# Kernel optimization log

Measured on AMD Instinct MI355X. Metric: run time of the kernel, lower is better.

Reference implementation:

```python
import jax, jax.numpy as jnp
import numpy as np

B, P = 65536, 22  # sets, max players per freeze frame
IN, HID, OUT = 6, 64, 128


def setup_inputs() -> dict:
    key = jax.random.key(0)
    k0, k1, k2, k3, k4, k5 = jax.random.split(key, 6)
    pitch = jnp.array([120.0, 80.0], dtype=jnp.float32)
    player_locs = jax.random.uniform(k0, (B, P, 2), dtype=jnp.float32) * pitch
    actor_locs = jax.random.uniform(k1, (B, 2), dtype=jnp.float32) * pitch
    # teammate / keeper flags in {0,1}
    flags = jax.random.randint(k2, (B, P, 2), 0, 2).astype(jnp.float32)
    # validity mask: 0 -> player skipped (simulates ragged / missing entries)
    mask = jax.random.randint(k3, (B, P), 0, 2).astype(jnp.int32)
    W1 = jax.random.normal(k4, (IN, HID), dtype=jnp.float32) / np.sqrt(IN)
    b1 = jnp.zeros((HID,), dtype=jnp.float32)
    W2 = jax.random.normal(k5, (HID, OUT), dtype=jnp.float32) / np.sqrt(HID)
    b2 = jnp.zeros((OUT,), dtype=jnp.float32)
    return {"player_locs": player_locs, "actor_locs": actor_locs, "flags": flags,
            "mask": mask, "W1": W1, "b1": b1, "W2": W2, "b2": b2}


def reference(player_locs, actor_locs, flags, mask, W1, b1, W2, b2):
    # per-player features relative to the actor: [dx, dy, dist, angle, teammate, keeper]
    dxy = player_locs - actor_locs[:, None, :]                 # [B,P,2]
    dist = jnp.sqrt(jnp.sum(dxy * dxy, axis=-1, keepdims=True))  # [B,P,1]
    angle = jnp.arctan2(dxy[..., 1:2], dxy[..., 0:1])            # [B,P,1]
    feats = jnp.concatenate([dxy, dist, angle, flags], axis=-1)  # [B,P,6]
    # PlayerMLP: Linear -> ReLU -> Linear
    h = jax.nn.relu(jnp.einsum('bpi,ih->bph', feats, W1) + b1)   # [B,P,64]
    emb = jnp.einsum('bph,ho->bpo', h, W2) + b2                  # [B,P,128]
    # masked mean over valid players; empty sets yield zeros (sum is 0)
    m = mask.astype(emb.dtype)[..., None]                        # [B,P,1]
    cnt = jnp.sum(m, axis=1)                                     # [B,1]
    pooled = jnp.sum(emb * m, axis=1) / jnp.maximum(cnt, 1.0)    # [B,128]
    return pooled
```

## Files before the change

### kernel.cpp

```cpp
#include <hip/hip_runtime.h>
#include <math.h>

#define PMAX 22
#define HID 64
#define OUTD 128
#define SETS_PER_WAVE 8
#define WAVES_PER_BLOCK 4

typedef __attribute__((ext_vector_type(4))) float float4v;
typedef _Float16 fh2 __attribute__((ext_vector_type(2)));
typedef _Float16 half8 __attribute__((ext_vector_type(8)));

__device__ __forceinline__ int rl_i(int v, int l) {
    return __builtin_amdgcn_readlane(v, l);
}
__device__ __forceinline__ int pk2(float x, float y) {
    auto v = __builtin_amdgcn_cvt_pkrtz(x, y);
    union { decltype(v) h; int i; } c;
    c.h = v;
    return c.i;
}
__device__ __forceinline__ unsigned short f16b(float x) {
    return (unsigned short)(pk2(x, x) & 0xFFFF);
}
__device__ __forceinline__ float fdot2i(int a, int b, float c) {
    union { int i; fh2 h; } ua, ub;
    ua.i = a;
    ub.i = b;
#if defined(__has_builtin) && __has_builtin(__builtin_amdgcn_fdot2)
    return __builtin_amdgcn_fdot2(ua.h, ub.h, c, false);
#else
    return fmaf((float)ua.h.x, (float)ub.h.x, fmaf((float)ua.h.y, (float)ub.h.y, c));
#endif
}
__device__ __forceinline__ void wave_lds_sync() {
    asm volatile("s_waitcnt lgkmcnt(0)" ::: "memory");
    __builtin_amdgcn_wave_barrier();
}
__device__ __forceinline__ float fast_atan2(float y, float x) {
    float ax = fabsf(x), ay = fabsf(y);
    float mn = fminf(ax, ay), mx = fmaxf(ax, ay);
    float a = mn * __builtin_amdgcn_rcpf(fmaxf(mx, 1e-30f));
    float s = a * a;
    float r = a * fmaf(s, fmaf(s, fmaf(s, -0.0851330f, 0.1801410f), -0.3302995f), 0.9998660f);
    if (ay > ax) r = 1.57079637f - r;
    if (x < 0.0f) r = 3.14159274f - r;
    return copysignf(r, y);
}

__global__ __launch_bounds__(256) void set_encoder_kernel(
    const float* __restrict__ player_locs,
    const float* __restrict__ actor_locs,
    const float* __restrict__ flags,
    const int*   __restrict__ mask,
    const float* __restrict__ W1,
    const float* __restrict__ b1,
    const float* __restrict__ W2,
    const float* __restrict__ b2,
    float* __restrict__ out)
{
    __shared__ __align__(16) unsigned w2f[16 * 256];
    __shared__ __align__(16) unsigned short hb[WAVES_PER_BLOCK][SETS_PER_WAVE][72];

    const int tid  = threadIdx.x;
    const int lane = tid & 63;
    const int wave = tid >> 6;

    const int wave_id = blockIdx.x * WAVES_PER_BLOCK + wave;
    const int set0    = wave_id * SETS_PER_WAVE;

    {
        const int pr = tid >> 3;
        const int nt = tid & 7;
        const float* rA = W2 + (size_t)(2 * pr) * OUTD + 16 * nt;
        const float* rB = rA + OUTD;
        float ra[16], rb[16];
#pragma unroll
        for (int i = 0; i < 4; ++i) {
            *(float4*)&ra[4 * i] = ((const float4*)rA)[i];
            *(float4*)&rb[4 * i] = ((const float4*)rB)[i];
        }
        const int kt = pr >> 4;
        const int kk = (2 * pr) & 31;
        const int Q  = kk >> 3;
        const int j2 = (kk >> 1) & 3;
        const int base = ((kt * 8 + nt) * 4 + Q) * 64 + j2;
#pragma unroll
        for (int c = 0; c < 16; ++c)
            w2f[base + 4 * c] = pk2(ra[c], rb[c]);
    }

    const int w01 = pk2(W1[0 * HID + lane], W1[1 * HID + lane]);
    const int w23 = pk2(W1[2 * HID + lane], W1[3 * HID + lane]);
    const int w45 = pk2(W1[4 * HID + lane], W1[5 * HID + lane]);
    const float b1l = b1[lane];

    __syncthreads();

    int fh[4][3];
    unsigned long long wbm[4];
    {
        const int lidx = lane < 2 * PMAX ? lane : 2 * PMAX - 1;
        const size_t r0 = (size_t)set0 * PMAX + lidx;
        const float2* plb = (const float2*)player_locs + r0;
        const float2* flb = (const float2*)flags + r0;
        const int*    mkb = mask + r0;
        const float2* acb = (const float2*)actor_locs + set0 + (lidx >= PMAX ? 1 : 0);
#pragma unroll
        for (int g = 0; g < 4; ++g) {
            float2 pl = plb[g * 2 * PMAX];
            float2 fl = flb[g * 2 * PMAX];
            int    m  = mkb[g * 2 * PMAX];
            float2 ac = acb[2 * g];
            float dx = pl.x - ac.x;
            float dy = pl.y - ac.y;
            float dist = __builtin_amdgcn_sqrtf(fmaf(dx, dx, dy * dy));
            float ang  = fast_atan2(dy, dx);
            fh[g][0] = pk2(dx, dy);
            fh[g][1] = pk2(dist, ang);
            fh[g][2] = pk2(fl.x, fl.y);
            unsigned long long bl = __ballot((lane < 2 * PMAX) && (m != 0));
            const unsigned lo = __builtin_amdgcn_readfirstlane((unsigned)bl);
            const unsigned hi = __builtin_amdgcn_readfirstlane((unsigned)(bl >> 32));
            wbm[g] = ((unsigned long long)hi << 32) | lo;
        }
    }

    unsigned nonempty = 0;
#pragma unroll
    for (int s = 0; s < SETS_PER_WAVE; ++s) {
        const int g    = s >> 1;
        const int base = (s & 1) * PMAX;
        const unsigned bits = (unsigned)(wbm[g] >> base) & 0x3FFFFFu;
        const int cnt = __builtin_popcount(bits);
        if (bits) nonempty |= (1u << s);
        float acc = 0.0f;
#pragma unroll
        for (int p = 0; p < PMAX; ++p) {
            if (bits & (1u << p)) {
                float t = fdot2i(rl_i(fh[g][0], base + p), w01, b1l);
                t = fdot2i(rl_i(fh[g][1], base + p), w23, t);
                t = fdot2i(rl_i(fh[g][2], base + p), w45, t);
                acc += fmaxf(t, 0.0f);
            }
        }
        const float hbar = acc * (1.0f / fmaxf((float)cnt, 1.0f));
        hb[wave][s][lane] = f16b(hbar);
    }
    wave_lds_sync();

    const int Q   = lane >> 4;
    const int c15 = lane & 15;
    const int sA  = lane & 7;
    half8 afrag[2];
#pragma unroll
    for (int kt = 0; kt < 2; ++kt) {
        union { uint4 u4; half8 h8; } cv;
        cv.u4 = *(const uint4*)&hb[wave][sA][kt * 32 + Q * 8];
        afrag[kt] = cv.h8;
    }

    float4v acc[8];
#pragma unroll
    for (int nt = 0; nt < 8; ++nt) {
        union { uint4 u4; half8 h8; } f0, f1;
        f0.u4 = *(const uint4*)&w2f[(0 * 8 + nt) * 256 + 4 * lane];
        f1.u4 = *(const uint4*)&w2f[(1 * 8 + nt) * 256 + 4 * lane];
        float4v z = {0.0f, 0.0f, 0.0f, 0.0f};
        acc[nt] = __builtin_amdgcn_mfma_f32_16x16x32_f16(afrag[0], f0.h8, z, 0, 0, 0);
        acc[nt] = __builtin_amdgcn_mfma_f32_16x16x32_f16(afrag[1], f1.h8, acc[nt], 0, 0, 0);
    }

    if (Q < 2) {
        float fs[4];
#pragma unroll
        for (int r = 0; r < 4; ++r) fs[r] = (float)((nonempty >> (4 * Q + r)) & 1u);

        const float* b2b = b2 + c15;
        float b2v[8];
#pragma unroll
        for (int nt = 0; nt < 8; ++nt) b2v[nt] = b2b[16 * nt];

        float* obase = out + (size_t)(set0 + 4 * Q) * OUTD + c15;
#pragma unroll
        for (int nt = 0; nt < 8; ++nt) {
#pragma unroll
            for (int r = 0; r < 4; ++r)
                obase[r * OUTD + nt * 16] = fmaf(fs[r], b2v[nt], acc[nt][r]);
        }
    }
}

extern "C" void kernel_launch(void* const* d_in, const int* in_sizes, int n_in,
                              void* d_out, int out_size, void* d_ws, size_t ws_size,
                              hipStream_t stream) {
    const float* player_locs = (const float*)d_in[0];
    const float* actor_locs  = (const float*)d_in[1];
    const float* flags       = (const float*)d_in[2];
    const int*   mask        = (const int*)d_in[3];
    const float* W1          = (const float*)d_in[4];
    const float* b1          = (const float*)d_in[5];
    const float* W2          = (const float*)d_in[6];
    const float* b2          = (const float*)d_in[7];
    float*       out         = (float*)d_out;

    const int B = in_sizes[0] / (PMAX * 2);
    const int sets_per_block = WAVES_PER_BLOCK * SETS_PER_WAVE;
    const int grid = (B + sets_per_block - 1) / sets_per_block;

    hipLaunchKernelGGL(set_encoder_kernel, dim3(grid), dim3(256), 0, stream,
                       player_locs, actor_locs, flags, mask, W1, b1, W2, b2, out);
}
```

Measured before the change: 110.4 us.

## Process two set groups per wave with prefetch of next group's inputs

Each wave now handles two groups of 8 sets in a loop instead of one. The block count is halved, so the per-block W2 LDS staging and W1 setup are amortized over twice as many sets. The next group's inputs are loaded into registers before the current group is computed, to overlap global loads with compute. The cost is higher register pressure and fewer blocks in flight, which can reduce latency hiding.

```diff
diff --git a/kernel.cpp b/kernel.cpp
--- a/kernel.cpp
+++ b/kernel.cpp
@@ -6,6 +6,7 @@
 #define OUTD 128
 #define SETS_PER_WAVE 8
 #define WAVES_PER_BLOCK 4
+#define GROUPS 2
 
 typedef __attribute__((ext_vector_type(4))) float float4v;
 typedef _Float16 fh2 __attribute__((ext_vector_type(2)));
@@ -66,8 +67,9 @@
     const int lane = tid & 63;
     const int wave = tid >> 6;
 
-    const int wave_id = blockIdx.x * WAVES_PER_BLOCK + wave;
-    const int set0    = wave_id * SETS_PER_WAVE;
+    const int wave_set_base =
+        blockIdx.x * (WAVES_PER_BLOCK * SETS_PER_WAVE * GROUPS) +
+        wave * (SETS_PER_WAVE * GROUPS);
 
     {
         const int pr = tid >> 3;
@@ -97,96 +99,114 @@
 
     __syncthreads();
 
-    int fh[4][3];
-    unsigned long long wbm[4];
-    {
-        const int lidx = lane < 2 * PMAX ? lane : 2 * PMAX - 1;
-        const size_t r0 = (size_t)set0 * PMAX + lidx;
+    const int lidx  = lane < 2 * PMAX ? lane : 2 * PMAX - 1;
+    const int acoff = (lidx >= PMAX ? 1 : 0);
+
+    float2 pl[2][4], fl[2][4], ac[2][4];
+    int    mk[2][4];
+    auto load_group = [&](int it, int buf) {
+        const int s0 = wave_set_base + it * SETS_PER_WAVE;
+        const size_t r0 = (size_t)s0 * PMAX + lidx;
         const float2* plb = (const float2*)player_locs + r0;
         const float2* flb = (const float2*)flags + r0;
         const int*    mkb = mask + r0;
-        const float2* acb = (const float2*)actor_locs + set0 + (lidx >= PMAX ? 1 : 0);
+        const float2* acb = (const float2*)actor_locs + s0 + acoff;
 #pragma unroll
         for (int g = 0; g < 4; ++g) {
-            float2 pl = plb[g * 2 * PMAX];
-            float2 fl = flb[g * 2 * PMAX];
-            int    m  = mkb[g * 2 * PMAX];
-            float2 ac = acb[2 * g];
-            float dx = pl.x - ac.x;
-            float dy = pl.y - ac.y;
+            pl[buf][g] = plb[g * 2 * PMAX];
+            fl[buf][g] = flb[g * 2 * PMAX];
+            mk[buf][g] = mkb[g * 2 * PMAX];
+            ac[buf][g] = acb[2 * g];
+        }
+    };
+    load_group(0, 0);
+
+    const int Q   = lane >> 4;
+    const int c15 = lane & 15;
+    const int sA  = lane & 7;
+    const float* b2b = b2 + c15;
+    float b2v[8];
+#pragma unroll
+    for (int nt = 0; nt < 8; ++nt) b2v[nt] = b2b[16 * nt];
+
+#pragma unroll
+    for (int it = 0; it < GROUPS; ++it) {
+        const int buf = it & 1;
+        if (it + 1 < GROUPS) load_group(it + 1, buf ^ 1);
+
+        const int set0 = wave_set_base + it * SETS_PER_WAVE;
+
+        int fh[4][3];
+        unsigned long long wbm[4];
+#pragma unroll
+        for (int g = 0; g < 4; ++g) {
+            float dx = pl[buf][g].x - ac[buf][g].x;
+            float dy = pl[buf][g].y - ac[buf][g].y;
             float dist = __builtin_amdgcn_sqrtf(fmaf(dx, dx, dy * dy));
             float ang  = fast_atan2(dy, dx);
             fh[g][0] = pk2(dx, dy);
             fh[g][1] = pk2(dist, ang);
-            fh[g][2] = pk2(fl.x, fl.y);
-            unsigned long long bl = __ballot((lane < 2 * PMAX) && (m != 0));
+            fh[g][2] = pk2(fl[buf][g].x, fl[buf][g].y);
+            unsigned long long bl = __ballot((lane < 2 * PMAX) && (mk[buf][g] != 0));
             const unsigned lo = __builtin_amdgcn_readfirstlane((unsigned)bl);
             const unsigned hi = __builtin_amdgcn_readfirstlane((unsigned)(bl >> 32));
             wbm[g] = ((unsigned long long)hi << 32) | lo;
         }
-    }
-
-    unsigned nonempty = 0;
-#pragma unroll
-    for (int s = 0; s < SETS_PER_WAVE; ++s) {
-        const int g    = s >> 1;
-        const int base = (s & 1) * PMAX;
-        const unsigned bits = (unsigned)(wbm[g] >> base) & 0x3FFFFFu;
-        const int cnt = __builtin_popcount(bits);
-        if (bits) nonempty |= (1u << s);
-        float acc = 0.0f;
-#pragma unroll
-        for (int p = 0; p < PMAX; ++p) {
-            if (bits & (1u << p)) {
-                float t = fdot2i(rl_i(fh[g][0], base + p), w01, b1l);
-                t = fdot2i(rl_i(fh[g][1], base + p), w23, t);
-                t = fdot2i(rl_i(fh[g][2], base + p), w45, t);
-                acc += fmaxf(t, 0.0f);
+
+        unsigned nonempty = 0;
+#pragma unroll
+        for (int s = 0; s < SETS_PER_WAVE; ++s) {
+            const int g    = s >> 1;
+            const int base = (s & 1) * PMAX;
+            const unsigned bits = (unsigned)(wbm[g] >> base) & 0x3FFFFFu;
+            const int cnt = __builtin_popcount(bits);
+            if (bits) nonempty |= (1u << s);
+            float acc = 0.0f;
+#pragma unroll
+            for (int p = 0; p < PMAX; ++p) {
+                if (bits & (1u << p)) {
+                    float t = fdot2i(rl_i(fh[g][0], base + p), w01, b1l);
+                    t = fdot2i(rl_i(fh[g][1], base + p), w23, t);
+                    t = fdot2i(rl_i(fh[g][2], base + p), w45, t);
+                    acc += fmaxf(t, 0.0f);
+                }
             }
-        }
-        const float hbar = acc * (1.0f / fmaxf((float)cnt, 1.0f));
-        hb[wave][s][lane] = f16b(hbar);
-    }
-    wave_lds_sync();
-
-    const int Q   = lane >> 4;
-    const int c15 = lane & 15;
-    const int sA  = lane & 7;
-    half8 afrag[2];
-#pragma unroll
-    for (int kt = 0; kt < 2; ++kt) {
-        union { uint4 u4; half8 h8; } cv;
-        cv.u4 = *(const uint4*)&hb[wave][sA][kt * 32 + Q * 8];
-        afrag[kt] = cv.h8;
-    }
-
-    float4v acc[8];
-#pragma unroll
-    for (int nt = 0; nt < 8; ++nt) {
-        union { uint4 u4; half8 h8; } f0, f1;
-        f0.u4 = *(const uint4*)&w2f[(0 * 8 + nt) * 256 + 4 * lane];
-        f1.u4 = *(const uint4*)&w2f[(1 * 8 + nt) * 256 + 4 * lane];
-        float4v z = {0.0f, 0.0f, 0.0f, 0.0f};
-        acc[nt] = __builtin_amdgcn_mfma_f32_16x16x32_f16(afrag[0], f0.h8, z, 0, 0, 0);
-        acc[nt] = __builtin_amdgcn_mfma_f32_16x16x32_f16(afrag[1], f1.h8, acc[nt], 0, 0, 0);
-    }
-
-    if (Q < 2) {
-        float fs[4];
-#pragma unroll
-        for (int r = 0; r < 4; ++r) fs[r] = (float)((nonempty >> (4 * Q + r)) & 1u);
-
-        const float* b2b = b2 + c15;
-        float b2v[8];
-#pragma unroll
-        for (int nt = 0; nt < 8; ++nt) b2v[nt] = b2b[16 * nt];
-
-        float* obase = out + (size_t)(set0 + 4 * Q) * OUTD + c15;
+            const float hbar = acc * (1.0f / fmaxf((float)cnt, 1.0f));
+            hb[wave][s][lane] = f16b(hbar);
+        }
+        wave_lds_sync();
+
+        half8 afrag[2];
+#pragma unroll
+        for (int kt = 0; kt < 2; ++kt) {
+            union { uint4 u4; half8 h8; } cv;
+            cv.u4 = *(const uint4*)&hb[wave][sA][kt * 32 + Q * 8];
+            afrag[kt] = cv.h8;
+        }
+
+        float4v acc[8];
 #pragma unroll
         for (int nt = 0; nt < 8; ++nt) {
-#pragma unroll
-            for (int r = 0; r < 4; ++r)
-                obase[r * OUTD + nt * 16] = fmaf(fs[r], b2v[nt], acc[nt][r]);
+            union { uint4 u4; half8 h8; } f0, f1;
+            f0.u4 = *(const uint4*)&w2f[(0 * 8 + nt) * 256 + 4 * lane];
+            f1.u4 = *(const uint4*)&w2f[(1 * 8 + nt) * 256 + 4 * lane];
+            float4v z = {0.0f, 0.0f, 0.0f, 0.0f};
+            acc[nt] = __builtin_amdgcn_mfma_f32_16x16x32_f16(afrag[0], f0.h8, z, 0, 0, 0);
+            acc[nt] = __builtin_amdgcn_mfma_f32_16x16x32_f16(afrag[1], f1.h8, acc[nt], 0, 0, 0);
+        }
+
+        if (Q < 2) {
+            float fs[4];
+#pragma unroll
+            for (int r = 0; r < 4; ++r) fs[r] = (float)((nonempty >> (4 * Q + r)) & 1u);
+
+            float* obase = out + (size_t)(set0 + 4 * Q) * OUTD + c15;
+#pragma unroll
+            for (int nt = 0; nt < 8; ++nt) {
+#pragma unroll
+                for (int r = 0; r < 4; ++r)
+                    obase[r * OUTD + nt * 16] = fmaf(fs[r], b2v[nt], acc[nt][r]);
+            }
         }
     }
 }
@@ -205,7 +225,7 @@
     float*       out         = (float*)d_out;
 
     const int B = in_sizes[0] / (PMAX * 2);
-    const int sets_per_block = WAVES_PER_BLOCK * SETS_PER_WAVE;
+    const int sets_per_block = WAVES_PER_BLOCK * SETS_PER_WAVE * GROUPS;
     const int grid = (B + sets_per_block - 1) / sets_per_block;
 
     hipLaunchKernelGGL(set_encoder_kernel, dim3(grid), dim3(256), 0, stream,
```

Result: slower. 113.9 us (+3.2%).

## Compute first MLP layer and masked pooling with MFMA instead of readlane dot2

Applied to the files above, without the earlier changes.

Replaces the per-set scalar loop, which broadcast each player's features with readlane and ran fdot2 for layer 1, with MFMA tiles. Player features are staged in LDS, layer 1 plus bias (folded in as a constant-1 column) runs as 16x16x32 f16 MFMAs, and ReLU outputs go to LDS as fp16. A second MFMA then multiplies a per-set mask matrix by these hidden values to do the masked sum. This removes the long serial readlane/dot chain but adds LDS traffic, extra shared memory per block, and wasted MFMA work, since the K dimension is mostly zero padding.

```diff
diff --git a/kernel.cpp b/kernel.cpp
--- a/kernel.cpp
+++ b/kernel.cpp
@@ -6,32 +6,22 @@
 #define OUTD 128
 #define SETS_PER_WAVE 8
 #define WAVES_PER_BLOCK 4
+#define ROWS 176
+#define ROWS_PAD 192
 
 typedef __attribute__((ext_vector_type(4))) float float4v;
-typedef _Float16 fh2 __attribute__((ext_vector_type(2)));
 typedef _Float16 half8 __attribute__((ext_vector_type(8)));
 
-__device__ __forceinline__ int rl_i(int v, int l) {
-    return __builtin_amdgcn_readlane(v, l);
-}
-__device__ __forceinline__ int pk2(float x, float y) {
+union U4 { uint4 u4; half8 h8; unsigned u[4]; };
+
+__device__ __forceinline__ unsigned pk2(float x, float y) {
     auto v = __builtin_amdgcn_cvt_pkrtz(x, y);
-    union { decltype(v) h; int i; } c;
+    union { decltype(v) h; unsigned i; } c;
     c.h = v;
     return c.i;
 }
 __device__ __forceinline__ unsigned short f16b(float x) {
     return (unsigned short)(pk2(x, x) & 0xFFFF);
-}
-__device__ __forceinline__ float fdot2i(int a, int b, float c) {
-    union { int i; fh2 h; } ua, ub;
-    ua.i = a;
-    ub.i = b;
-#if defined(__has_builtin) && __has_builtin(__builtin_amdgcn_fdot2)
-    return __builtin_amdgcn_fdot2(ua.h, ub.h, c, false);
-#else
-    return fmaf((float)ua.h.x, (float)ub.h.x, fmaf((float)ua.h.y, (float)ub.h.y, c));
-#endif
 }
 __device__ __forceinline__ void wave_lds_sync() {
     asm volatile("s_waitcnt lgkmcnt(0)" ::: "memory");
@@ -60,14 +50,21 @@
     float* __restrict__ out)
 {
     __shared__ __align__(16) unsigned w2f[16 * 256];
+    __shared__ __align__(16) unsigned feats[WAVES_PER_BLOCK * ROWS_PAD * 4];
+    __shared__ __align__(16) unsigned Hl[WAVES_PER_BLOCK * 64 * 20];
     __shared__ __align__(16) unsigned short hb[WAVES_PER_BLOCK][SETS_PER_WAVE][72];
 
     const int tid  = threadIdx.x;
     const int lane = tid & 63;
     const int wave = tid >> 6;
+    const int Q    = lane >> 4;
+    const int c15  = lane & 15;
 
     const int wave_id = blockIdx.x * WAVES_PER_BLOCK + wave;
     const int set0    = wave_id * SETS_PER_WAVE;
+
+    unsigned* featw = &feats[wave * ROWS_PAD * 4];
+    unsigned* Hw    = &Hl[wave * 64 * 20];
 
     {
         const int pr = tid >> 3;
@@ -82,22 +79,31 @@
         }
         const int kt = pr >> 4;
         const int kk = (2 * pr) & 31;
-        const int Q  = kk >> 3;
+        const int q  = kk >> 3;
         const int j2 = (kk >> 1) & 3;
-        const int base = ((kt * 8 + nt) * 4 + Q) * 64 + j2;
+        const int base = ((kt * 8 + nt) * 4 + q) * 64 + j2;
 #pragma unroll
         for (int c = 0; c < 16; ++c)
             w2f[base + 4 * c] = pk2(ra[c], rb[c]);
     }
 
-    const int w01 = pk2(W1[0 * HID + lane], W1[1 * HID + lane]);
-    const int w23 = pk2(W1[2 * HID + lane], W1[3 * HID + lane]);
-    const int w45 = pk2(W1[4 * HID + lane], W1[5 * HID + lane]);
-    const float b1l = b1[lane];
+    U4 w1f[4];
+#pragma unroll
+    for (int nt = 0; nt < 4; ++nt) {
+        const int col = 16 * nt + c15;
+        const bool q0 = (Q == 0);
+        float a0 = W1[0 * HID + col], a1 = W1[1 * HID + col];
+        float a2 = W1[2 * HID + col], a3 = W1[3 * HID + col];
+        float a4 = W1[4 * HID + col], a5 = W1[5 * HID + col];
+        float bb = b1[col];
+        w1f[nt].u[0] = q0 ? pk2(a0, a1) : 0u;
+        w1f[nt].u[1] = q0 ? pk2(a2, a3) : 0u;
+        w1f[nt].u[2] = q0 ? pk2(a4, a5) : 0u;
+        w1f[nt].u[3] = q0 ? pk2(bb, 0.f) : 0u;
+    }
 
     __syncthreads();
 
-    int fh[4][3];
     unsigned long long wbm[4];
     {
         const int lidx = lane < 2 * PMAX ? lane : 2 * PMAX - 1;
@@ -116,46 +122,111 @@
             float dy = pl.y - ac.y;
             float dist = __builtin_amdgcn_sqrtf(fmaf(dx, dx, dy * dy));
             float ang  = fast_atan2(dy, dx);
-            fh[g][0] = pk2(dx, dy);
-            fh[g][1] = pk2(dist, ang);
-            fh[g][2] = pk2(fl.x, fl.y);
+            if (lane < 2 * PMAX) {
+                uint4 v;
+                v.x = pk2(dx, dy);
+                v.y = pk2(dist, ang);
+                v.z = pk2(fl.x, fl.y);
+                v.w = pk2(1.0f, 0.f);
+                *(uint4*)&featw[(g * 44 + lane) * 4] = v;
+            }
             unsigned long long bl = __ballot((lane < 2 * PMAX) && (m != 0));
             const unsigned lo = __builtin_amdgcn_readfirstlane((unsigned)bl);
             const unsigned hi = __builtin_amdgcn_readfirstlane((unsigned)(bl >> 32));
             wbm[g] = ((unsigned long long)hi << 32) | lo;
         }
     }
-
+    if (lane < 16) {
+        uint4 z = {0u, 0u, 0u, 0u};
+        *(uint4*)&featw[(ROWS + lane) * 4] = z;
+    }
+    wave_lds_sync();
+
+    unsigned bm32[6];
+    {
+        unsigned long long t0 = wbm[0] | (wbm[1] << 44);
+        unsigned long long t1 = (wbm[1] >> 20) | (wbm[2] << 24);
+        unsigned long long t2 = (wbm[2] >> 40) | (wbm[3] << 4);
+        bm32[0] = (unsigned)t0; bm32[1] = (unsigned)(t0 >> 32);
+        bm32[2] = (unsigned)t1; bm32[3] = (unsigned)(t1 >> 32);
+        bm32[4] = (unsigned)t2; bm32[5] = (unsigned)(t2 >> 32);
+    }
     unsigned nonempty = 0;
-#pragma unroll
-    for (int s = 0; s < SETS_PER_WAVE; ++s) {
-        const int g    = s >> 1;
-        const int base = (s & 1) * PMAX;
-        const unsigned bits = (unsigned)(wbm[g] >> base) & 0x3FFFFFu;
-        const int cnt = __builtin_popcount(bits);
+    float rcpc[8];
+#pragma unroll
+    for (int s = 0; s < 8; ++s) {
+        unsigned bits = (unsigned)(wbm[s >> 1] >> ((s & 1) * PMAX)) & 0x3FFFFFu;
+        int cnt = __builtin_popcount(bits);
         if (bits) nonempty |= (1u << s);
-        float acc = 0.0f;
-#pragma unroll
-        for (int p = 0; p < PMAX; ++p) {
-            if (bits & (1u << p)) {
-                float t = fdot2i(rl_i(fh[g][0], base + p), w01, b1l);
-                t = fdot2i(rl_i(fh[g][1], base + p), w23, t);
-                t = fdot2i(rl_i(fh[g][2], base + p), w45, t);
-                acc += fmaxf(t, 0.0f);
+        rcpc[s] = 1.0f / (float)(cnt > 0 ? cnt : 1);
+    }
+
+    float4v pacc[4];
+#pragma unroll
+    for (int nt = 0; nt < 4; ++nt) pacc[nt] = (float4v){0.f, 0.f, 0.f, 0.f};
+
+    const int vd0 = 8 * Q - PMAX * c15;
+
+#pragma unroll
+    for (int kt = 0; kt < 6; ++kt) {
+#pragma unroll
+        for (int i = 0; i < 2; ++i) {
+            const int tt = 2 * kt + i;
+            const int arow = (Q == 0) ? (16 * tt + c15) : (ROWS + c15);
+            U4 av;
+            av.u4 = *(const uint4*)&featw[arow * 4];
+#pragma unroll
+            for (int nt = 0; nt < 4; ++nt) {
+                float4v z = {0.f, 0.f, 0.f, 0.f};
+                float4v c1 = __builtin_amdgcn_mfma_f32_16x16x32_f16(av.h8, w1f[nt].h8, z, 0, 0, 0);
+                uint2 wv;
+                wv.x = pk2(fmaxf(c1[0], 0.f), fmaxf(c1[1], 0.f));
+                wv.y = pk2(fmaxf(c1[2], 0.f), fmaxf(c1[3], 0.f));
+                *(uint2*)&Hw[(16 * nt + c15) * 20 + 8 * i + 2 * Q] = wv;
             }
         }
-        const float hbar = acc * (1.0f / fmaxf((float)cnt, 1.0f));
-        hb[wave][s][lane] = f16b(hbar);
+        wave_lds_sync();
+
+        unsigned bits8 = (bm32[kt] >> (8 * Q)) & 0xFFu;
+        const int d = vd0 + 32 * kt;
+        unsigned rp = 0x3FFFFFu >> (d & 31);
+        unsigned rn = 0x3FFFFFu << ((-d) & 31);
+        unsigned rm = (d >= 0) ? rp : rn;
+        rm = (d >= 22) ? 0u : rm;
+        rm = (d <= -8) ? 0u : rm;
+        unsigned m8 = bits8 & rm;
+        U4 mf;
+#pragma unroll
+        for (int j2 = 0; j2 < 4; ++j2) {
+            unsigned b = (m8 >> (2 * j2)) & 3u;
+            mf.u[j2] = ((b & 1u) ? 0x00003C00u : 0u) | ((b & 2u) ? 0x3C000000u : 0u);
+        }
+
+#pragma unroll
+        for (int nt = 0; nt < 4; ++nt) {
+            U4 bv;
+            bv.u4 = *(const uint4*)&Hw[(16 * nt + c15) * 20 + 4 * Q];
+            pacc[nt] = __builtin_amdgcn_mfma_f32_16x16x32_f16(mf.h8, bv.h8, pacc[nt], 0, 0, 0);
+        }
+        wave_lds_sync();
+    }
+
+    if (Q < 2) {
+#pragma unroll
+        for (int r = 0; r < 4; ++r) {
+            const float rc = Q ? rcpc[4 + r] : rcpc[r];
+#pragma unroll
+            for (int nt = 0; nt < 4; ++nt)
+                hb[wave][4 * Q + r][16 * nt + c15] = f16b(pacc[nt][r] * rc);
+        }
     }
     wave_lds_sync();
 
-    const int Q   = lane >> 4;
-    const int c15 = lane & 15;
-    const int sA  = lane & 7;
+    const int sA = lane & 7;
     half8 afrag[2];
 #pragma unroll
     for (int kt = 0; kt < 2; ++kt) {
-        union { uint4 u4; half8 h8; } cv;
+        U4 cv;
         cv.u4 = *(const uint4*)&hb[wave][sA][kt * 32 + Q * 8];
         afrag[kt] = cv.h8;
     }
@@ -163,10 +234,10 @@
     float4v acc[8];
 #pragma unroll
     for (int nt = 0; nt < 8; ++nt) {
-        union { uint4 u4; half8 h8; } f0, f1;
+        U4 f0, f1;
         f0.u4 = *(const uint4*)&w2f[(0 * 8 + nt) * 256 + 4 * lane];
         f1.u4 = *(const uint4*)&w2f[(1 * 8 + nt) * 256 + 4 * lane];
-        float4v z = {0.0f, 0.0f, 0.0f, 0.0f};
+        float4v z = {0.f, 0.f, 0.f, 0.f};
         acc[nt] = __builtin_amdgcn_mfma_f32_16x16x32_f16(afrag[0], f0.h8, z, 0, 0, 0);
         acc[nt] = __builtin_amdgcn_mfma_f32_16x16x32_f16(afrag[1], f1.h8, acc[nt], 0, 0, 0);
     }
```

New measurement: 122.7 us. 1.11x slower.
